# Optimization experiments

Hardware: AMD Instinct MI355X
Metric: run time of the kernel (lower is better)

The kernel has to match this reference:

```python
import jax, jax.numpy as jnp
import numpy as np

N_ITEMS = 100000
LATDIM = 128
KNN_K = 5
NUM_GCN_LAYERS = 2


def setup_inputs() -> dict:
    key = jax.random.key(0)
    k1, k2 = jax.random.split(key)
    item_rep = jax.random.normal(k1, (N_ITEMS, LATDIM), dtype=jnp.float32)
    knn_ind = jax.random.randint(k2, (N_ITEMS, KNN_K), 0, N_ITEMS, dtype=jnp.int32)
    return {"item_rep": item_rep, "knn_ind": knn_ind}


def reference(item_rep, knn_ind):
    # item_rep: [N, D], knn_ind: [N, K] column indices of the KNN adjacency.
    N, K = knn_ind.shape
    # compute_normalized_laplacian: adjacency has value 1 at (i, knn_ind[i,k]).
    # row_sum[i] = K (exactly K ones per row from topk) + 1e-7 eps.
    row_sum = jnp.full((N,), float(K), dtype=item_rep.dtype) + 1e-7
    r_inv_sqrt = row_sum ** -0.5                      # [N]
    vals = r_inv_sqrt[:, None] * r_inv_sqrt[knn_ind]  # [N, K] edge weights

    # forward: item_embs = [item_rep]; repeated SpMM; return sum of all layers.
    x = item_rep
    acc = x
    for _ in range(NUM_GCN_LAYERS):
        # fixed-degree SpMM: out[n] = sum_k vals[n,k] * x[knn_ind[n,k]]
        x = jnp.einsum('nk,nkd->nd', vals, x[knn_ind])
        acc = acc + x
    return acc
```

## Files before the change

kernel.cpp:

```cpp
#include <hip/hip_runtime.h>
#include <math.h>


#define GCN_K 5
#define D4 32

typedef float f32x4 __attribute__((ext_vector_type(4)));

static __device__ __forceinline__ ushort f2bf(float f) {
  unsigned u = __float_as_uint(f);
  u = (u + 0x7fffu + ((u >> 16) & 1u)) >> 16;
  return (ushort)u;
}
static __device__ __forceinline__ float bf2f(ushort u) {
  return __uint_as_float(((unsigned)u) << 16);
}

__global__ __launch_bounds__(256) void gcn_layer1(
    const float4* __restrict__ x0, const int* __restrict__ knn,
    ushort4* __restrict__ x1, float w, int n) {
  int t = blockIdx.x * 256 + threadIdx.x;
  int row = t >> 5;
  if (row >= n) return;
  int c = t & 31;
  const int* kp = knn + row * GCN_K;
  float4 s = make_float4(0.f, 0.f, 0.f, 0.f);
#pragma unroll
  for (int k = 0; k < GCN_K; ++k) {
    int j = kp[k];
    float4 v = x0[(size_t)j * D4 + c];
    s.x += v.x; s.y += v.y; s.z += v.z; s.w += v.w;
  }
  ushort4 p;
  p.x = f2bf(w * s.x); p.y = f2bf(w * s.y);
  p.z = f2bf(w * s.z); p.w = f2bf(w * s.w);
  x1[(size_t)row * D4 + c] = p;
}

__global__ __launch_bounds__(256) void gcn_layer2(
    const float4* __restrict__ x0, const ushort4* __restrict__ x1,
    const int* __restrict__ knn, float* __restrict__ out, float w, int n) {
  int t = blockIdx.x * 256 + threadIdx.x;
  int row = t >> 5;
  if (row >= n) return;
  int c = t & 31;
  const int* kp = knn + row * GCN_K;
  float4 s = make_float4(0.f, 0.f, 0.f, 0.f);
#pragma unroll
  for (int k = 0; k < GCN_K; ++k) {
    int j = kp[k];
    ushort4 v = x1[(size_t)j * D4 + c];
    s.x += bf2f(v.x); s.y += bf2f(v.y); s.z += bf2f(v.z); s.w += bf2f(v.w);
  }
  float4 a = x0[(size_t)row * D4 + c];
  ushort4 bq = x1[(size_t)row * D4 + c];
  f32x4 o;
  o.x = a.x + bf2f(bq.x) + w * s.x;
  o.y = a.y + bf2f(bq.y) + w * s.y;
  o.z = a.z + bf2f(bq.z) + w * s.z;
  o.w = a.w + bf2f(bq.w) + w * s.w;
  f32x4* op = (f32x4*)(out + ((size_t)row * D4 + c) * 4);
  __builtin_nontemporal_store(o, op);
}

extern "C" void kernel_launch(void* const* d_in, const int* in_sizes, int n_in,
                              void* d_out, int out_size, void* d_ws, size_t ws_size,
                              hipStream_t stream) {
  const float* x0 = (const float*)d_in[0];
  const int* knn = (const int*)d_in[1];
  float* out = (float*)d_out;
  ushort4* x1 = (ushort4*)d_ws;

  int n = in_sizes[0] / 128;

  float r = powf(5.0f + 1e-7f, -0.5f);
  float w = r * r;

  int total = n * 32;
  int blocks = (total + 255) / 256;
  gcn_layer1<<<blocks, 256, 0, stream>>>((const float4*)x0, knn, x1, w, n);
  gcn_layer2<<<blocks, 256, 0, stream>>>((const float4*)x0, x1, knn,
                                         out, w, n);
}
```

Before: 152.0 us.

## Pre-convert input to bf16 and gather 16-byte vectors with 16 threads per row

Adds a conversion kernel that writes a bf16 copy of item_rep, so layer 1 gathers half as many bytes per neighbor row. Both layers now use 16 threads per row, each loading 8 bf16 values as one 16-byte vector. The cost is an extra launch plus a full read of the fp32 input and a write of the bf16 copy. Layer 1 also loses precision because it now sums rounded inputs.

```diff
diff --git a/kernel.cpp b/kernel.cpp
--- a/kernel.cpp
+++ b/kernel.cpp
@@ -3,9 +3,9 @@
 
 
 #define GCN_K 5
-#define D4 32
 
 typedef float f32x4 __attribute__((ext_vector_type(4)));
+typedef ushort u16x8 __attribute__((ext_vector_type(8)));
 
 static __device__ __forceinline__ ushort f2bf(float f) {
   unsigned u = __float_as_uint(f);
@@ -16,51 +16,71 @@
   return __uint_as_float(((unsigned)u) << 16);
 }
 
+__global__ __launch_bounds__(256) void cvt_bf16(
+    const f32x4* __restrict__ x0, u16x8* __restrict__ y0, int n8) {
+  int t = blockIdx.x * 256 + threadIdx.x;
+  if (t >= n8) return;
+  f32x4 a = x0[2 * t];
+  f32x4 b = x0[2 * t + 1];
+  u16x8 p;
+  p[0] = f2bf(a.x); p[1] = f2bf(a.y); p[2] = f2bf(a.z); p[3] = f2bf(a.w);
+  p[4] = f2bf(b.x); p[5] = f2bf(b.y); p[6] = f2bf(b.z); p[7] = f2bf(b.w);
+  y0[t] = p;
+}
+
 __global__ __launch_bounds__(256) void gcn_layer1(
-    const float4* __restrict__ x0, const int* __restrict__ knn,
-    ushort4* __restrict__ x1, float w, int n) {
+    const u16x8* __restrict__ y0, const int* __restrict__ knn,
+    u16x8* __restrict__ x1, float w, int n) {
   int t = blockIdx.x * 256 + threadIdx.x;
-  int row = t >> 5;
+  int row = t >> 4;
   if (row >= n) return;
-  int c = t & 31;
+  int c = t & 15;
   const int* kp = knn + row * GCN_K;
-  float4 s = make_float4(0.f, 0.f, 0.f, 0.f);
+  float s[8] = {0.f, 0.f, 0.f, 0.f, 0.f, 0.f, 0.f, 0.f};
 #pragma unroll
   for (int k = 0; k < GCN_K; ++k) {
     int j = kp[k];
-    float4 v = x0[(size_t)j * D4 + c];
-    s.x += v.x; s.y += v.y; s.z += v.z; s.w += v.w;
+    u16x8 v = y0[(size_t)j * 16 + c];
+#pragma unroll
+    for (int e = 0; e < 8; ++e) s[e] += bf2f(v[e]);
   }
-  ushort4 p;
-  p.x = f2bf(w * s.x); p.y = f2bf(w * s.y);
-  p.z = f2bf(w * s.z); p.w = f2bf(w * s.w);
-  x1[(size_t)row * D4 + c] = p;
+  u16x8 p;
+#pragma unroll
+  for (int e = 0; e < 8; ++e) p[e] = f2bf(w * s[e]);
+  x1[(size_t)row * 16 + c] = p;
 }
 
 __global__ __launch_bounds__(256) void gcn_layer2(
-    const float4* __restrict__ x0, const ushort4* __restrict__ x1,
+    const f32x4* __restrict__ x0, const u16x8* __restrict__ x1,
     const int* __restrict__ knn, float* __restrict__ out, float w, int n) {
   int t = blockIdx.x * 256 + threadIdx.x;
-  int row = t >> 5;
+  int row = t >> 4;
   if (row >= n) return;
-  int c = t & 31;
+  int c = t & 15;
   const int* kp = knn + row * GCN_K;
-  float4 s = make_float4(0.f, 0.f, 0.f, 0.f);
+  float s[8] = {0.f, 0.f, 0.f, 0.f, 0.f, 0.f, 0.f, 0.f};
 #pragma unroll
   for (int k = 0; k < GCN_K; ++k) {
     int j = kp[k];
-    ushort4 v = x1[(size_t)j * D4 + c];
-    s.x += bf2f(v.x); s.y += bf2f(v.y); s.z += bf2f(v.z); s.w += bf2f(v.w);
+    u16x8 v = x1[(size_t)j * 16 + c];
+#pragma unroll
+    for (int e = 0; e < 8; ++e) s[e] += bf2f(v[e]);
   }
-  float4 a = x0[(size_t)row * D4 + c];
-  ushort4 bq = x1[(size_t)row * D4 + c];
-  f32x4 o;
-  o.x = a.x + bf2f(bq.x) + w * s.x;
-  o.y = a.y + bf2f(bq.y) + w * s.y;
-  o.z = a.z + bf2f(bq.z) + w * s.z;
-  o.w = a.w + bf2f(bq.w) + w * s.w;
-  f32x4* op = (f32x4*)(out + ((size_t)row * D4 + c) * 4);
-  __builtin_nontemporal_store(o, op);
+  f32x4 a0 = x0[(size_t)row * 32 + 2 * c];
+  f32x4 a1 = x0[(size_t)row * 32 + 2 * c + 1];
+  u16x8 b = x1[(size_t)row * 16 + c];
+  f32x4 o0, o1;
+  o0.x = a0.x + bf2f(b[0]) + w * s[0];
+  o0.y = a0.y + bf2f(b[1]) + w * s[1];
+  o0.z = a0.z + bf2f(b[2]) + w * s[2];
+  o0.w = a0.w + bf2f(b[3]) + w * s[3];
+  o1.x = a1.x + bf2f(b[4]) + w * s[4];
+  o1.y = a1.y + bf2f(b[5]) + w * s[5];
+  o1.z = a1.z + bf2f(b[6]) + w * s[6];
+  o1.w = a1.w + bf2f(b[7]) + w * s[7];
+  f32x4* op = (f32x4*)(out + (size_t)row * 128 + c * 8);
+  __builtin_nontemporal_store(o0, op);
+  __builtin_nontemporal_store(o1, op + 1);
 }
 
 extern "C" void kernel_launch(void* const* d_in, const int* in_sizes, int n_in,
@@ -69,16 +89,17 @@
   const float* x0 = (const float*)d_in[0];
   const int* knn = (const int*)d_in[1];
   float* out = (float*)d_out;
-  ushort4* x1 = (ushort4*)d_ws;
 
   int n = in_sizes[0] / 128;
+  u16x8* y0 = (u16x8*)d_ws;
+  u16x8* x1 = (u16x8*)((char*)d_ws + (size_t)n * 128 * 2);
 
   float r = powf(5.0f + 1e-7f, -0.5f);
   float w = r * r;
 
-  int total = n * 32;
-  int blocks = (total + 255) / 256;
-  gcn_layer1<<<blocks, 256, 0, stream>>>((const float4*)x0, knn, x1, w, n);
-  gcn_layer2<<<blocks, 256, 0, stream>>>((const float4*)x0, x1, knn,
-                                         out, w, n);
+  int n8 = n * 16;
+  int blocks = (n8 + 255) / 256;
+  cvt_bf16<<<blocks, 256, 0, stream>>>((const f32x4*)x0, y0, n8);
+  gcn_layer1<<<blocks, 256, 0, stream>>>(y0, knn, x1, w, n);
+  gcn_layer2<<<blocks, 256, 0, stream>>>((const f32x4*)x0, x1, knn, out, w, n);
 }
```

After: 150.3 us. No clear change (-1.1%).
